# Kernel optimization log

Measured on AMD Instinct MI355X. Metric: run time of the kernel, lower is better.

## Reference

```python
import jax, jax.numpy as jnp
import numpy as np

N, Wd = 1000000, 20
EPS = 1e-16


def setup_inputs() -> dict:
    key = jax.random.key(0)
    ks = jax.random.split(key, 40)
    def rn(i, shape, scale=0.05):
        return jax.random.normal(ks[i], shape, dtype=jnp.float32) * scale
    inp = {
        "X": rn(0, (1, 14), 1.0),
        "read_weights": jax.nn.sigmoid(rn(1, (1, N), 1.0)),
        "write_weights": jax.nn.sigmoid(rn(2, (1, N), 1.0)),
        "Memory": jnp.full((N, Wd), 1e-6, dtype=jnp.float32),
        "read_head": jax.nn.sigmoid(rn(3, (1, Wd), 1.0)),
        "W1": rn(4, (48, 14)), "b1": rn(5, (48,)),
        "W2": rn(6, (72, 48)), "b2": rn(7, (72,)),
        "Wxi": rn(8, ((Wd + 6) * 2 + 2 * Wd, 72)), "bxi": rn(9, ((Wd + 6) * 2 + 2 * Wd,)),
        "Wz": rn(10, (3, 72)), "bz": rn(11, (3,)),
        "Wv": rn(12, (20, 325)), "bv": rn(13, (20,)),
        "aW1": rn(14, (110, 40)), "ab1": rn(15, (110,)),
        "aW2": rn(16, (190, 110)), "ab2": rn(17, (190,)),
        "aW3": rn(18, (270, 190)), "ab3": rn(19, (270,)),
        "aW4": rn(20, (325, 270)), "ab4": rn(21, (325,)),
        "mW1": rn(22, (110, 40)), "mb1": rn(23, (110,)),
        "mW2": rn(24, (190, 110)), "mb2": rn(25, (190,)),
        "mW3": rn(26, (270, 190)), "mb3": rn(27, (270,)),
        "mW4": rn(28, (325, 270)), "mb4": rn(29, (325,)),
    }
    return inp


def _alu(x, W1, b1, W2, b2, W3, b3, W4, b4):
    x = jax.nn.relu(x @ W1.T + b1)
    x = jax.nn.relu(x @ W2.T + b2)
    x = jax.nn.relu(x @ W3.T + b3)
    return jax.nn.softmax(x @ W4.T + b4, axis=-1)


def _head_params(p):  # p: (1, Wd+6)
    k = jnp.tanh(p[0, :Wd])[None, :]              # (1, Wd)
    g = jax.nn.sigmoid(p[0, Wd])
    s = jax.nn.softmax(p[0, Wd + 1:Wd + 4])        # (3,)
    gamma = 1.0 + jax.nn.softplus(p[0, Wd + 4])
    beta = jax.nn.softplus(p[0, Wd + 5])
    return k, g, s, gamma, beta


def _address(Memory, k, beta, g, s, gamma, w_prev):
    Me = Memory + EPS                              # (N, Wd)
    ke = k + EPS                                   # (1, Wd)
    num = (Me @ ke.T)[:, 0]                        # (N,)
    den = jnp.maximum(jnp.linalg.norm(Me, axis=-1), 1e-8) * \
          jnp.maximum(jnp.linalg.norm(ke, axis=-1), 1e-8)
    w_c = jax.nn.softmax((num / den) * beta)       # (N,)
    w_g = g * w_c + (1.0 - g) * w_prev             # (1, N)
    pad = jnp.concatenate([w_g[:, -1:], w_g, w_g[:, :1]], axis=1)  # (1, N+2)
    w_r = s[0] * pad[:, :N] + s[1] * pad[:, 1:N + 1] + s[2] * pad[:, 2:]
    w = w_r ** gamma
    return w / (jnp.sum(w, axis=1, keepdims=True) + EPS)


def reference(X, read_weights, write_weights, Memory, read_head,
              W1, b1, W2, b2, Wxi, bxi, Wz, bz, Wv, bv,
              aW1, ab1, aW2, ab2, aW3, ab3, aW4, ab4,
              mW1, mb1, mW2, mb2, mW3, mb3, mW4, mb4):
    h = X @ W1.T + b1                # (1, 48)  (no activation, faithful)
    h = h @ W2.T + b2                # (1, 72)
    xi = h @ Wxi.T + bxi             # (1, 92)
    zeta = h @ Wz.T + bz             # (1, 3)

    rp = xi[0, :Wd + 6][None, :]
    wp = xi[0, Wd + 6:(Wd + 6) * 2][None, :]
    erase = jax.nn.sigmoid(xi[0, (Wd + 6) * 2:(Wd + 6) * 2 + Wd][None, :])
    add = jnp.tanh(xi[0, (Wd + 6) * 2 + Wd:(Wd + 6) * 2 + 2 * Wd][None, :])

    k, g, s, gamma, beta = _head_params(rp)
    rw = _address(Memory, k, beta, g, s, gamma, read_weights)
    k, g, s, gamma, beta = _head_params(wp)
    ww = _address(Memory, k, beta, g, s, gamma, write_weights)

    new_read_head = rw @ Memory                    # (1, Wd)
    alu_in = jnp.concatenate([read_head, new_read_head], axis=1)  # (1, 2*Wd)

    rho = jax.nn.sigmoid(zeta[0, 0])
    alu_head = jax.nn.softmax(zeta[:, 1:], axis=-1)  # (1, 2)
    out_add = _alu(alu_in, aW1, ab1, aW2, ab2, aW3, ab3, aW4, ab4)
    out_mul = _alu(alu_in, mW1, mb1, mW2, mb2, mW3, mb3, mW4, mb4)
    out = alu_head[0, 0] * out_add + alu_head[0, 1] * out_mul  # (1, 325)

    v = out @ Wv.T + bv                              # (1, 20)
    add = rho * add + (1.0 - rho) * v

    new_memory = Memory * (1.0 - ww.T @ erase) + ww.T @ add  # (N, Wd)
    return out, rw, ww, new_memory, new_read_head
```

## Files before the change

kernel.cpp:

```cpp
#include <hip/hip_runtime.h>
#include <math.h>

#define NN 1000000
#define WD 20
#define NB 977
#define PST 1024

#define OUT_OFF 0
#define RW_OFF  325
#define WW_OFF  1000325
#define NM_OFF  2000325
#define NRH_OFF 22000325

__device__ __forceinline__ float sigmoidf_(float x){ return 1.0f/(1.0f+expf(-x)); }
__device__ __forceinline__ float softplusf_(float x){ return (x>30.f)?x:log1pf(expf(x)); }

__global__ void k_head(const float* __restrict__ X,
                       const float* __restrict__ W1, const float* __restrict__ b1,
                       const float* __restrict__ W2, const float* __restrict__ b2,
                       const float* __restrict__ Wxi, const float* __restrict__ bxi,
                       const float* __restrict__ Wz, const float* __restrict__ bz,
                       float* __restrict__ P){
  __shared__ float h1[48], h2[72], xi[92], zeta[3];
  int t = threadIdx.x;
  if(t<48){ float a=b1[t]; const float* w=W1+t*14; for(int c=0;c<14;c++) a+=X[c]*w[c]; h1[t]=a; }
  __syncthreads();
  if(t<72){ float a=b2[t]; const float* w=W2+t*48; for(int c=0;c<48;c++) a+=h1[c]*w[c]; h2[t]=a; }
  __syncthreads();
  if(t<92){ float a=bxi[t]; const float* w=Wxi+t*72; for(int c=0;c<72;c++) a+=h2[c]*w[c]; xi[t]=a; }
  else if(t<95){ int z=t-92; float a=bz[z]; const float* w=Wz+z*72; for(int c=0;c<72;c++) a+=h2[c]*w[c]; zeta[z]=a; }
  __syncthreads();
  if(t<20){
    P[0+t]  = tanhf(xi[t]);
    P[32+t] = tanhf(xi[26+t]);
    P[64+t] = sigmoidf_(xi[52+t]);
    P[84+t] = tanhf(xi[72+t]);
  }
  if(t==32){
    const float* p = xi;
    float g=sigmoidf_(p[20]);
    float a0=p[21],a1=p[22],a2=p[23];
    float mx=fmaxf(a0,fmaxf(a1,a2));
    float e0=expf(a0-mx),e1=expf(a1-mx),e2=expf(a2-mx),es=e0+e1+e2;
    float gamma=1.0f+softplusf_(p[24]);
    float beta=softplusf_(p[25]);
    float n2=0.f; for(int j=0;j<20;j++){ float ke=tanhf(p[j])+1e-16f; n2+=ke*ke; }
    P[20]=g; P[21]=e0/es; P[22]=e1/es; P[23]=e2/es; P[24]=gamma; P[25]=beta;
    P[26]=fmaxf(sqrtf(n2),1e-8f);
  }
  if(t==33){
    const float* p = xi+26;
    float g=sigmoidf_(p[20]);
    float a0=p[21],a1=p[22],a2=p[23];
    float mx=fmaxf(a0,fmaxf(a1,a2));
    float e0=expf(a0-mx),e1=expf(a1-mx),e2=expf(a2-mx),es=e0+e1+e2;
    float gamma=1.0f+softplusf_(p[24]);
    float beta=softplusf_(p[25]);
    float n2=0.f; for(int j=0;j<20;j++){ float ke=tanhf(p[j])+1e-16f; n2+=ke*ke; }
    P[52]=g; P[53]=e0/es; P[54]=e1/es; P[55]=e2/es; P[56]=gamma; P[57]=beta;
    P[58]=fmaxf(sqrtf(n2),1e-8f);
  }
  if(t==34){
    P[104]=sigmoidf_(zeta[0]);
    float mx=fmaxf(zeta[1],zeta[2]);
    float e1=expf(zeta[1]-mx), e2=expf(zeta[2]-mx);
    P[105]=e1/(e1+e2); P[106]=e2/(e1+e2);
  }
}

__global__ __launch_bounds__(256) void k_scores(const float* __restrict__ M, const float* __restrict__ P,
                         float* __restrict__ score_r, float* __restrict__ score_w,
                         float4* __restrict__ pms){
  int t=threadIdx.x, b=blockIdx.x;
  float kr[20], kw[20];
#pragma unroll
  for(int j=0;j<20;j++){ kr[j]=P[j]+1e-16f; kw[j]=P[32+j]+1e-16f; }
  float betar=P[25], betaw=P[57], knr=P[26], knw=P[58];
  float sR[4], sW[4];
#pragma unroll
  for(int p=0;p<4;p++){
    int i=b*1024+p*256+t;
    if(i<NN){
      const float4* row=(const float4*)(M+(size_t)i*WD);
      float dr=0.f,dw=0.f,n2=0.f;
#pragma unroll
      for(int q=0;q<5;q++){
        float4 v=row[q];
        float m0=v.x+1e-16f,m1=v.y+1e-16f,m2=v.z+1e-16f,m3=v.w+1e-16f;
        dr+=m0*kr[4*q]+m1*kr[4*q+1]+m2*kr[4*q+2]+m3*kr[4*q+3];
        dw+=m0*kw[4*q]+m1*kw[4*q+1]+m2*kw[4*q+2]+m3*kw[4*q+3];
        n2+=m0*m0+m1*m1+m2*m2+m3*m3;
      }
      float nm=fmaxf(sqrtf(n2),1e-8f);
      sR[p]=betar*(dr/(nm*knr));
      sW[p]=betaw*(dw/(nm*knw));
      score_r[i]=sR[p]; score_w[i]=sW[p];
    } else { sR[p]=-3.0e38f; sW[p]=-3.0e38f; }
  }
  __shared__ float r1[256], r2[256];
  __shared__ double d1[256], d2[256];
  float lm1=fmaxf(fmaxf(sR[0],sR[1]),fmaxf(sR[2],sR[3]));
  float lm2=fmaxf(fmaxf(sW[0],sW[1]),fmaxf(sW[2],sW[3]));
  r1[t]=lm1; r2[t]=lm2; __syncthreads();
  for(int o=128;o>0;o>>=1){ if(t<o){ r1[t]=fmaxf(r1[t],r1[t+o]); r2[t]=fmaxf(r2[t],r2[t+o]); } __syncthreads(); }
  float mb1=r1[0], mb2=r2[0]; __syncthreads();
  double s1=0.0,s2=0.0;
#pragma unroll
  for(int p=0;p<4;p++){ s1+=(double)expf(sR[p]-mb1); s2+=(double)expf(sW[p]-mb2); }
  d1[t]=s1; d2[t]=s2; __syncthreads();
  for(int o=128;o>0;o>>=1){ if(t<o){ d1[t]+=d1[t+o]; d2[t]+=d2[t+o]; } __syncthreads(); }
  if(t==0) pms[b]=make_float4(mb1,mb2,(float)d1[0],(float)d2[0]);
}

__global__ __launch_bounds__(256) void k_shift(const float* __restrict__ score_r, const float* __restrict__ score_w,
                        const float* __restrict__ wpr, const float* __restrict__ wpw,
                        const float* __restrict__ M, const float* __restrict__ P,
                        const float4* __restrict__ pms,
                        float* __restrict__ w_r_out, float* __restrict__ w_w_out,
                        double* __restrict__ pZ, double* __restrict__ pnrhT){
  __shared__ float r1[256], r2[256];
  __shared__ double d1[256], d2[256];
  __shared__ float bmS[4];
  __shared__ float wsum[4][20];
  int t=threadIdx.x, b=blockIdx.x;
  float4 v[4];
#pragma unroll
  for(int k=0;k<4;k++){
    int idx=t+k*256;
    v[k] = (idx<NB) ? pms[idx] : make_float4(-3.0e38f,-3.0e38f,0.f,0.f);
  }
  float lm1=fmaxf(fmaxf(v[0].x,v[1].x),fmaxf(v[2].x,v[3].x));
  float lm2=fmaxf(fmaxf(v[0].y,v[1].y),fmaxf(v[2].y,v[3].y));
  r1[t]=lm1; r2[t]=lm2; __syncthreads();
  for(int o=128;o>0;o>>=1){ if(t<o){ r1[t]=fmaxf(r1[t],r1[t+o]); r2[t]=fmaxf(r2[t],r2[t+o]); } __syncthreads(); }
  if(t==0){ bmS[0]=r1[0]; bmS[1]=r2[0]; } __syncthreads();
  float mr=bmS[0], mw=bmS[1];
  double s1=0.0,s2=0.0;
#pragma unroll
  for(int k=0;k<4;k++){
    s1 += (double)v[k].z * (double)expf(v[k].x-mr);
    s2 += (double)v[k].w * (double)expf(v[k].y-mw);
  }
  d1[t]=s1; d2[t]=s2; __syncthreads();
  for(int o=128;o>0;o>>=1){ if(t<o){ d1[t]+=d1[t+o]; d2[t]+=d2[t+o]; } __syncthreads(); }
  if(t==0){ bmS[2]=(float)d1[0]; bmS[3]=(float)d2[0]; } __syncthreads();
  float Sr=bmS[2], Sw=bmS[3];
  float gr=P[20], s0r=P[21], s1r=P[22], s2r=P[23], gar=P[24];
  float gw=P[52], s0w=P[53], s1w=P[54], s2w=P[55], gaw=P[56];
  float omgr=1.0f-gr, omgw=1.0f-gw;
  float acc[20];
#pragma unroll
  for(int j=0;j<20;j++) acc[j]=0.f;
  double zr=0.0, zw=0.0;
  for(int p=0;p<4;p++){
    int i=b*1024+p*256+t;
    if(i<NN){
      int im1=(i==0)?(NN-1):(i-1);
      int ip1=(i==NN-1)?0:(i+1);
      float wgrm = gr*(expf(score_r[im1]-mr)/Sr) + omgr*wpr[im1];
      float wgr0 = gr*(expf(score_r[i  ]-mr)/Sr) + omgr*wpr[i  ];
      float wgrp = gr*(expf(score_r[ip1]-mr)/Sr) + omgr*wpr[ip1];
      float wgwm = gw*(expf(score_w[im1]-mw)/Sw) + omgw*wpw[im1];
      float wgw0 = gw*(expf(score_w[i  ]-mw)/Sw) + omgw*wpw[i  ];
      float wgwp = gw*(expf(score_w[ip1]-mw)/Sw) + omgw*wpw[ip1];
      float wr = powf(s0r*wgrm + s1r*wgr0 + s2r*wgrp, gar);
      float ww = powf(s0w*wgwm + s1w*wgw0 + s2w*wgwp, gaw);
      w_r_out[i]=wr; w_w_out[i]=ww;
      zr+=(double)wr; zw+=(double)ww;
      const float4* row=(const float4*)(M+(size_t)i*WD);
#pragma unroll
      for(int q=0;q<5;q++){
        float4 mv=row[q];
        acc[4*q+0]+=wr*mv.x; acc[4*q+1]+=wr*mv.y; acc[4*q+2]+=wr*mv.z; acc[4*q+3]+=wr*mv.w;
      }
    }
  }
  d1[t]=zr; d2[t]=zw; __syncthreads();
  for(int o=128;o>0;o>>=1){ if(t<o){ d1[t]+=d1[t+o]; d2[t]+=d2[t+o]; } __syncthreads(); }
  if(t==0){ pZ[2*b]=d1[0]; pZ[2*b+1]=d2[0]; }
#pragma unroll
  for(int j=0;j<20;j++){
    for(int off=32;off>0;off>>=1) acc[j]+=__shfl_down(acc[j],off,64);
  }
  int wave=t>>6, lane=t&63;
  if(lane==0){
#pragma unroll
    for(int j=0;j<20;j++) wsum[wave][j]=acc[j];
  }
  __syncthreads();
  if(t<20){
    double s=(double)wsum[0][t]+(double)wsum[1][t]+(double)wsum[2][t]+(double)wsum[3][t];
    pnrhT[(size_t)t*PST+b]=s;
  }
}

__global__ __launch_bounds__(256) void k_nrh(const double* __restrict__ pZ, const double* __restrict__ pnrhT,
                      const float* __restrict__ read_head,
                      float* __restrict__ in40, float* __restrict__ out, double* __restrict__ Sd){
  __shared__ double dd[256];
  __shared__ double bZ[2];
  int t=threadIdx.x, j=blockIdx.x;
  double a=0.0,c=0.0;
  for(int idx=t; idx<NB; idx+=256){ a+=pZ[2*idx]; c+=pZ[2*idx+1]; }
  dd[t]=a; __syncthreads();
  for(int o=128;o>0;o>>=1){ if(t<o) dd[t]+=dd[t+o]; __syncthreads(); }
  if(t==0) bZ[0]=dd[0]; __syncthreads();
  dd[t]=c; __syncthreads();
  for(int o=128;o>0;o>>=1){ if(t<o) dd[t]+=dd[t+o]; __syncthreads(); }
  if(t==0) bZ[1]=dd[0]; __syncthreads();
  if(j==0 && t==0){ Sd[0]=bZ[0]; Sd[1]=bZ[1]; }
  double s=0.0;
  for(int idx=t; idx<NB; idx+=256) s+=pnrhT[(size_t)j*PST+idx];
  dd[t]=s; __syncthreads();
  for(int o=128;o>0;o>>=1){ if(t<o) dd[t]+=dd[t+o]; __syncthreads(); }
  if(t==0){
    float nv=(float)(dd[0]/(bZ[0]+1e-16));
    in40[20+j]=nv; out[NRH_OFF+j]=nv;
    in40[j]=read_head[j];
  }
}

__global__ __launch_bounds__(256) void k_layer(const float* __restrict__ Wa, const float* __restrict__ ba,
                        const float* __restrict__ Wm, const float* __restrict__ bm,
                        const float* __restrict__ inA, const float* __restrict__ inM,
                        float* __restrict__ oA, float* __restrict__ oM,
                        int rows, int K, int RB, int doRelu){
  int net = (blockIdx.x >= RB) ? 1 : 0;
  const float* W = net ? Wm : Wa;
  const float* bb = net ? bm : ba;
  const float* in = net ? inM : inA;
  float* o = net ? oM : oA;
  int wave=threadIdx.x>>6, lane=threadIdx.x&63;
  int r=(blockIdx.x - net*RB)*4 + wave;
  if(r>=rows) return;
  const float* w = W + (size_t)r*K;
  float a=0.f;
  for(int c=lane; c<K; c+=64) a += w[c]*in[c];
  for(int off=32;off>0;off>>=1) a += __shfl_down(a,off,64);
  if(lane==0){
    float vv=a+bb[r];
    o[r]= doRelu ? fmaxf(vv,0.f) : vv;
  }
}

__global__ __launch_bounds__(512) void k_fin(const float* __restrict__ h4a, const float* __restrict__ h4m,
                      const float* __restrict__ Wv, const float* __restrict__ bv,
                      float* __restrict__ P, float* __restrict__ out){
  __shared__ float red[512];
  __shared__ float A[325], B[325];
  __shared__ float sc[2];
  int t=threadIdx.x;
  float la=(t<325)?h4a[t]:-3.0e38f;
  red[t]=la; __syncthreads();
  for(int o=256;o>0;o>>=1){ if(t<o) red[t]=fmaxf(red[t],red[t+o]); __syncthreads(); }
  if(t==0) sc[0]=red[0]; __syncthreads();
  float ea=(t<325)?expf(la-sc[0]):0.f;
  red[t]=ea; __syncthreads();
  for(int o=256;o>0;o>>=1){ if(t<o) red[t]+=red[t+o]; __syncthreads(); }
  if(t==0) sc[1]=red[0]; __syncthreads();
  if(t<325) A[t]=ea/sc[1];
  __syncthreads();
  float lm=(t<325)?h4m[t]:-3.0e38f;
  red[t]=lm; __syncthreads();
  for(int o=256;o>0;o>>=1){ if(t<o) red[t]=fmaxf(red[t],red[t+o]); __syncthreads(); }
  if(t==0) sc[0]=red[0]; __syncthreads();
  float em=(t<325)?expf(lm-sc[0]):0.f;
  red[t]=em; __syncthreads();
  for(int o=256;o>0;o>>=1){ if(t<o) red[t]+=red[t+o]; __syncthreads(); }
  if(t==0) sc[1]=red[0]; __syncthreads();
  if(t<325) B[t]=em/sc[1];
  __syncthreads();
  float ah0=P[105], ah1=P[106];
  if(t<325){ float ov=ah0*A[t]+ah1*B[t]; out[OUT_OFF+t]=ov; A[t]=ov; }
  __syncthreads();
  int wave=t>>6, lane=t&63;
  for(int r=wave; r<20; r+=8){
    const float* w=Wv+(size_t)r*325;
    float a=0.f;
    for(int c=lane;c<325;c+=64) a+=w[c]*A[c];
    for(int off=32;off>0;off>>=1) a+=__shfl_down(a,off,64);
    if(lane==0){
      float vv=a+bv[r];
      float rho=P[104];
      P[112+r]=rho*P[84+r]+(1.0f-rho)*vv;
    }
  }
}

__global__ __launch_bounds__(256) void k_memupd(const float* __restrict__ M,
                         float* __restrict__ w_r, float* __restrict__ w_w,
                         const float* __restrict__ P, const double* __restrict__ Sd,
                         float* __restrict__ nm){
  int t=threadIdx.x, b=blockIdx.x;
  float er[20], af[20];
#pragma unroll
  for(int j=0;j<20;j++){ er[j]=P[64+j]; af[j]=P[112+j]; }
  float Zr=(float)Sd[0]+1e-16f, Zw=(float)Sd[1]+1e-16f;
  for(int p=0;p<4;p++){
    int i=b*1024+p*256+t;
    if(i<NN){
      float wrn=w_r[i]/Zr;
      float wwn=w_w[i]/Zw;
      w_r[i]=wrn; w_w[i]=wwn;
      const float4* row=(const float4*)(M+(size_t)i*WD);
      float4* dst=(float4*)(nm+(size_t)i*WD);
#pragma unroll
      for(int q=0;q<5;q++){
        float4 v=row[q];
        float4 o;
        o.x=v.x*(1.0f-wwn*er[4*q+0])+wwn*af[4*q+0];
        o.y=v.y*(1.0f-wwn*er[4*q+1])+wwn*af[4*q+1];
        o.z=v.z*(1.0f-wwn*er[4*q+2])+wwn*af[4*q+2];
        o.w=v.w*(1.0f-wwn*er[4*q+3])+wwn*af[4*q+3];
        dst[q]=o;
      }
    }
  }
}

extern "C" void kernel_launch(void* const* d_in, const int* in_sizes, int n_in,
                              void* d_out, int out_size, void* d_ws, size_t ws_size,
                              hipStream_t stream) {
  const float* X    =(const float*)d_in[0];
  const float* rwp  =(const float*)d_in[1];
  const float* wwp  =(const float*)d_in[2];
  const float* Mem  =(const float*)d_in[3];
  const float* rhd  =(const float*)d_in[4];
  const float* W1   =(const float*)d_in[5];
  const float* b1   =(const float*)d_in[6];
  const float* W2   =(const float*)d_in[7];
  const float* b2   =(const float*)d_in[8];
  const float* Wxi  =(const float*)d_in[9];
  const float* bxi  =(const float*)d_in[10];
  const float* Wz   =(const float*)d_in[11];
  const float* bz   =(const float*)d_in[12];
  const float* Wv   =(const float*)d_in[13];
  const float* bv   =(const float*)d_in[14];
  const float* aW1  =(const float*)d_in[15];
  const float* ab1  =(const float*)d_in[16];
  const float* aW2  =(const float*)d_in[17];
  const float* ab2  =(const float*)d_in[18];
  const float* aW3  =(const float*)d_in[19];
  const float* ab3  =(const float*)d_in[20];
  const float* aW4  =(const float*)d_in[21];
  const float* ab4  =(const float*)d_in[22];
  const float* mW1  =(const float*)d_in[23];
  const float* mb1  =(const float*)d_in[24];
  const float* mW2  =(const float*)d_in[25];
  const float* mb2  =(const float*)d_in[26];
  const float* mW3  =(const float*)d_in[27];
  const float* mb3  =(const float*)d_in[28];
  const float* mW4  =(const float*)d_in[29];
  const float* mb4  =(const float*)d_in[30];

  float* out = (float*)d_out;
  char* ws = (char*)d_ws;
  float*  P     = (float*) (ws + 0);
  float4* pms   = (float4*)(ws + 4096);
  double* pZ    = (double*)(ws + 32768);
  double* pnrhT = (double*)(ws + 65536);
  double* Sd    = (double*)(ws + 229376);
  float*  in40  = (float*) (ws + 229504);
  float*  F     = (float*) (ws + 229760);
  float *h1a=F,      *h1m=F+110;
  float *h2a=F+220,  *h2m=F+410;
  float *h3a=F+600,  *h3m=F+870;
  float *h4a=F+1140, *h4m=F+1465;

  float* score_r = out + NM_OFF;
  float* score_w = score_r + NN;
  float* w_r = out + RW_OFF;
  float* w_w = out + WW_OFF;
  float* nm  = out + NM_OFF;

  k_head<<<1,128,0,stream>>>(X,W1,b1,W2,b2,Wxi,bxi,Wz,bz,P);
  k_scores<<<NB,256,0,stream>>>(Mem,P,score_r,score_w,pms);
  k_shift<<<NB,256,0,stream>>>(score_r,score_w,rwp,wwp,Mem,P,pms,w_r,w_w,pZ,pnrhT);
  k_nrh<<<20,256,0,stream>>>(pZ,pnrhT,rhd,in40,out,Sd);
  k_layer<<<56,256,0,stream>>>(aW1,ab1,mW1,mb1,in40,in40,h1a,h1m,110,40,28,1);
  k_layer<<<96,256,0,stream>>>(aW2,ab2,mW2,mb2,h1a,h1m,h2a,h2m,190,110,48,1);
  k_layer<<<136,256,0,stream>>>(aW3,ab3,mW3,mb3,h2a,h2m,h3a,h3m,270,190,68,1);
  k_layer<<<164,256,0,stream>>>(aW4,ab4,mW4,mb4,h3a,h3m,h4a,h4m,325,270,82,0);
  k_fin<<<1,512,0,stream>>>(h4a,h4m,Wv,bv,P,out);
  k_memupd<<<NB,256,0,stream>>>(Mem,w_r,w_w,P,Sd,nm);
}
```

Before: 120.5 us.

## Stage memory rows through LDS, interleave scores, fuse MLP chain with grid barriers

Memory rows are now loaded cooperatively as coalesced float4 tiles into shared memory in the scores, shift and update kernels, replacing per-thread strided 80-byte row reads. The update kernel also writes its output back through LDS. Read and write scores are stored interleaved as float2, so the shift stencil fetches both with one load. The reduction, four MLP layers and final projection are merged into one persistent 96-block kernel using atomic global barriers, removing six launches at the risk of spin-wait cost and a deadlock if not all blocks are co-resident.

```diff
diff --git a/kernel.cpp b/kernel.cpp
--- a/kernel.cpp
+++ b/kernel.cpp
@@ -2,9 +2,11 @@
 #include <math.h>
 
 #define NN 1000000
+#define NF4 5000000
 #define WD 20
 #define NB 977
 #define PST 1024
+#define MLPB 96
 
 #define OUT_OFF 0
 #define RW_OFF  325
@@ -15,14 +17,25 @@
 __device__ __forceinline__ float sigmoidf_(float x){ return 1.0f/(1.0f+expf(-x)); }
 __device__ __forceinline__ float softplusf_(float x){ return (x>30.f)?x:log1pf(expf(x)); }
 
+__device__ __forceinline__ void gbar(unsigned* c, unsigned nb){
+  __syncthreads();
+  if(threadIdx.x==0){
+    __hip_atomic_fetch_add(c,1u,__ATOMIC_ACQ_REL,__HIP_MEMORY_SCOPE_AGENT);
+    while(__hip_atomic_load(c,__ATOMIC_ACQUIRE,__HIP_MEMORY_SCOPE_AGENT) < nb)
+      __builtin_amdgcn_s_sleep(8);
+  }
+  __syncthreads();
+}
+
 __global__ void k_head(const float* __restrict__ X,
                        const float* __restrict__ W1, const float* __restrict__ b1,
                        const float* __restrict__ W2, const float* __restrict__ b2,
                        const float* __restrict__ Wxi, const float* __restrict__ bxi,
                        const float* __restrict__ Wz, const float* __restrict__ bz,
-                       float* __restrict__ P){
+                       float* __restrict__ P, unsigned* __restrict__ cnt){
   __shared__ float h1[48], h2[72], xi[92], zeta[3];
   int t = threadIdx.x;
+  if(t>=96 && t<112) cnt[t-96]=0u;
   if(t<48){ float a=b1[t]; const float* w=W1+t*14; for(int c=0;c<14;c++) a+=X[c]*w[c]; h1[t]=a; }
   __syncthreads();
   if(t<72){ float a=b2[t]; const float* w=W2+t*48; for(int c=0;c<48;c++) a+=h1[c]*w[c]; h2[t]=a; }
@@ -69,36 +82,46 @@
 }
 
 __global__ __launch_bounds__(256) void k_scores(const float* __restrict__ M, const float* __restrict__ P,
-                         float* __restrict__ score_r, float* __restrict__ score_w,
-                         float4* __restrict__ pms){
+                         float2* __restrict__ sc2, float4* __restrict__ pms){
+  __shared__ float4 ld[1280];
   int t=threadIdx.x, b=blockIdx.x;
   float kr[20], kw[20];
 #pragma unroll
   for(int j=0;j<20;j++){ kr[j]=P[j]+1e-16f; kw[j]=P[32+j]+1e-16f; }
   float betar=P[25], betaw=P[57], knr=P[26], knw=P[58];
+  const float4* Mf4=(const float4*)M;
   float sR[4], sW[4];
-#pragma unroll
   for(int p=0;p<4;p++){
-    int i=b*1024+p*256+t;
+    int rb=b*1024+p*256;
+    size_t f4b=(size_t)rb*5;
+#pragma unroll
+    for(int k=0;k<5;k++){
+      size_t idx=f4b+(size_t)(k*256+t);
+      ld[k*256+t] = (idx<NF4)?Mf4[idx]:make_float4(0.f,0.f,0.f,0.f);
+    }
+    __syncthreads();
+    int i=rb+t;
+    float srv=-3.0e38f, swv=-3.0e38f;
     if(i<NN){
-      const float4* row=(const float4*)(M+(size_t)i*WD);
       float dr=0.f,dw=0.f,n2=0.f;
 #pragma unroll
       for(int q=0;q<5;q++){
-        float4 v=row[q];
+        float4 v=ld[t*5+q];
         float m0=v.x+1e-16f,m1=v.y+1e-16f,m2=v.z+1e-16f,m3=v.w+1e-16f;
         dr+=m0*kr[4*q]+m1*kr[4*q+1]+m2*kr[4*q+2]+m3*kr[4*q+3];
         dw+=m0*kw[4*q]+m1*kw[4*q+1]+m2*kw[4*q+2]+m3*kw[4*q+3];
         n2+=m0*m0+m1*m1+m2*m2+m3*m3;
       }
       float nm=fmaxf(sqrtf(n2),1e-8f);
-      sR[p]=betar*(dr/(nm*knr));
-      sW[p]=betaw*(dw/(nm*knw));
-      score_r[i]=sR[p]; score_w[i]=sW[p];
-    } else { sR[p]=-3.0e38f; sW[p]=-3.0e38f; }
-  }
-  __shared__ float r1[256], r2[256];
-  __shared__ double d1[256], d2[256];
+      srv=betar*(dr/(nm*knr));
+      swv=betaw*(dw/(nm*knw));
+      sc2[i]=make_float2(srv,swv);
+    }
+    sR[p]=srv; sW[p]=swv;
+    __syncthreads();
+  }
+  float* r1=(float*)ld; float* r2=r1+256;
+  double* d1=(double*)(r1+512); double* d2=d1+256;
   float lm1=fmaxf(fmaxf(sR[0],sR[1]),fmaxf(sR[2],sR[3]));
   float lm2=fmaxf(fmaxf(sW[0],sW[1]),fmaxf(sW[2],sW[3]));
   r1[t]=lm1; r2[t]=lm2; __syncthreads();
@@ -112,25 +135,26 @@
   if(t==0) pms[b]=make_float4(mb1,mb2,(float)d1[0],(float)d2[0]);
 }
 
-__global__ __launch_bounds__(256) void k_shift(const float* __restrict__ score_r, const float* __restrict__ score_w,
+__global__ __launch_bounds__(256) void k_shift(const float2* __restrict__ sc2,
                         const float* __restrict__ wpr, const float* __restrict__ wpw,
                         const float* __restrict__ M, const float* __restrict__ P,
                         const float4* __restrict__ pms,
                         float* __restrict__ w_r_out, float* __restrict__ w_w_out,
                         double* __restrict__ pZ, double* __restrict__ pnrhT){
-  __shared__ float r1[256], r2[256];
-  __shared__ double d1[256], d2[256];
+  __shared__ float4 ld[1280];
   __shared__ float bmS[4];
-  __shared__ float wsum[4][20];
+  float* r1=(float*)ld; float* r2=r1+256;
+  double* d1=(double*)(r1+512); double* d2=d1+256;
+  float* wsum=(float*)(d2+256);
   int t=threadIdx.x, b=blockIdx.x;
-  float4 v[4];
+  float4 v4[4];
 #pragma unroll
   for(int k=0;k<4;k++){
     int idx=t+k*256;
-    v[k] = (idx<NB) ? pms[idx] : make_float4(-3.0e38f,-3.0e38f,0.f,0.f);
-  }
-  float lm1=fmaxf(fmaxf(v[0].x,v[1].x),fmaxf(v[2].x,v[3].x));
-  float lm2=fmaxf(fmaxf(v[0].y,v[1].y),fmaxf(v[2].y,v[3].y));
+    v4[k] = (idx<NB) ? pms[idx] : make_float4(-3.0e38f,-3.0e38f,0.f,0.f);
+  }
+  float lm1=fmaxf(fmaxf(v4[0].x,v4[1].x),fmaxf(v4[2].x,v4[3].x));
+  float lm2=fmaxf(fmaxf(v4[0].y,v4[1].y),fmaxf(v4[2].y,v4[3].y));
   r1[t]=lm1; r2[t]=lm2; __syncthreads();
   for(int o=128;o>0;o>>=1){ if(t<o){ r1[t]=fmaxf(r1[t],r1[t+o]); r2[t]=fmaxf(r2[t],r2[t+o]); } __syncthreads(); }
   if(t==0){ bmS[0]=r1[0]; bmS[1]=r2[0]; } __syncthreads();
@@ -138,8 +162,8 @@
   double s1=0.0,s2=0.0;
 #pragma unroll
   for(int k=0;k<4;k++){
-    s1 += (double)v[k].z * (double)expf(v[k].x-mr);
-    s2 += (double)v[k].w * (double)expf(v[k].y-mw);
+    s1 += (double)v4[k].z * (double)expf(v4[k].x-mr);
+    s2 += (double)v4[k].w * (double)expf(v4[k].y-mw);
   }
   d1[t]=s1; d2[t]=s2; __syncthreads();
   for(int o=128;o>0;o>>=1){ if(t<o){ d1[t]+=d1[t+o]; d2[t]+=d2[t+o]; } __syncthreads(); }
@@ -148,36 +172,47 @@
   float gr=P[20], s0r=P[21], s1r=P[22], s2r=P[23], gar=P[24];
   float gw=P[52], s0w=P[53], s1w=P[54], s2w=P[55], gaw=P[56];
   float omgr=1.0f-gr, omgw=1.0f-gw;
+  const float4* Mf4=(const float4*)M;
   float acc[20];
 #pragma unroll
   for(int j=0;j<20;j++) acc[j]=0.f;
   double zr=0.0, zw=0.0;
   for(int p=0;p<4;p++){
-    int i=b*1024+p*256+t;
+    int rb=b*1024+p*256;
+    size_t f4b=(size_t)rb*5;
+#pragma unroll
+    for(int k=0;k<5;k++){
+      size_t idx=f4b+(size_t)(k*256+t);
+      ld[k*256+t] = (idx<NF4)?Mf4[idx]:make_float4(0.f,0.f,0.f,0.f);
+    }
+    __syncthreads();
+    int i=rb+t;
     if(i<NN){
       int im1=(i==0)?(NN-1):(i-1);
       int ip1=(i==NN-1)?0:(i+1);
-      float wgrm = gr*(expf(score_r[im1]-mr)/Sr) + omgr*wpr[im1];
-      float wgr0 = gr*(expf(score_r[i  ]-mr)/Sr) + omgr*wpr[i  ];
-      float wgrp = gr*(expf(score_r[ip1]-mr)/Sr) + omgr*wpr[ip1];
-      float wgwm = gw*(expf(score_w[im1]-mw)/Sw) + omgw*wpw[im1];
-      float wgw0 = gw*(expf(score_w[i  ]-mw)/Sw) + omgw*wpw[i  ];
-      float wgwp = gw*(expf(score_w[ip1]-mw)/Sw) + omgw*wpw[ip1];
+      float2 scm=sc2[im1], sc0=sc2[i], scp=sc2[ip1];
+      float wgrm = gr*(expf(scm.x-mr)/Sr) + omgr*wpr[im1];
+      float wgr0 = gr*(expf(sc0.x-mr)/Sr) + omgr*wpr[i  ];
+      float wgrp = gr*(expf(scp.x-mr)/Sr) + omgr*wpr[ip1];
+      float wgwm = gw*(expf(scm.y-mw)/Sw) + omgw*wpw[im1];
+      float wgw0 = gw*(expf(sc0.y-mw)/Sw) + omgw*wpw[i  ];
+      float wgwp = gw*(expf(scp.y-mw)/Sw) + omgw*wpw[ip1];
       float wr = powf(s0r*wgrm + s1r*wgr0 + s2r*wgrp, gar);
       float ww = powf(s0w*wgwm + s1w*wgw0 + s2w*wgwp, gaw);
       w_r_out[i]=wr; w_w_out[i]=ww;
       zr+=(double)wr; zw+=(double)ww;
-      const float4* row=(const float4*)(M+(size_t)i*WD);
 #pragma unroll
       for(int q=0;q<5;q++){
-        float4 mv=row[q];
+        float4 mv=ld[t*5+q];
         acc[4*q+0]+=wr*mv.x; acc[4*q+1]+=wr*mv.y; acc[4*q+2]+=wr*mv.z; acc[4*q+3]+=wr*mv.w;
       }
     }
+    __syncthreads();
   }
   d1[t]=zr; d2[t]=zw; __syncthreads();
   for(int o=128;o>0;o>>=1){ if(t<o){ d1[t]+=d1[t+o]; d2[t]+=d2[t+o]; } __syncthreads(); }
   if(t==0){ pZ[2*b]=d1[0]; pZ[2*b+1]=d2[0]; }
+  __syncthreads();
 #pragma unroll
   for(int j=0;j<20;j++){
     for(int off=32;off>0;off>>=1) acc[j]+=__shfl_down(acc[j],off,64);
@@ -185,104 +220,143 @@
   int wave=t>>6, lane=t&63;
   if(lane==0){
 #pragma unroll
-    for(int j=0;j<20;j++) wsum[wave][j]=acc[j];
+    for(int j=0;j<20;j++) wsum[wave*20+j]=acc[j];
   }
   __syncthreads();
   if(t<20){
-    double s=(double)wsum[0][t]+(double)wsum[1][t]+(double)wsum[2][t]+(double)wsum[3][t];
+    double s=(double)wsum[0*20+t]+(double)wsum[1*20+t]+(double)wsum[2*20+t]+(double)wsum[3*20+t];
     pnrhT[(size_t)t*PST+b]=s;
   }
 }
 
-__global__ __launch_bounds__(256) void k_nrh(const double* __restrict__ pZ, const double* __restrict__ pnrhT,
+__global__ __launch_bounds__(256) void k_mlp(const double* __restrict__ pZ, const double* __restrict__ pnrhT,
                       const float* __restrict__ read_head,
-                      float* __restrict__ in40, float* __restrict__ out, double* __restrict__ Sd){
+                      const float* __restrict__ aW1,const float* __restrict__ ab1,
+                      const float* __restrict__ aW2,const float* __restrict__ ab2,
+                      const float* __restrict__ aW3,const float* __restrict__ ab3,
+                      const float* __restrict__ aW4,const float* __restrict__ ab4,
+                      const float* __restrict__ mW1,const float* __restrict__ mb1,
+                      const float* __restrict__ mW2,const float* __restrict__ mb2,
+                      const float* __restrict__ mW3,const float* __restrict__ mb3,
+                      const float* __restrict__ mW4,const float* __restrict__ mb4,
+                      const float* __restrict__ Wv, const float* __restrict__ bv,
+                      float* __restrict__ P, float* __restrict__ out,
+                      float* __restrict__ in40, float* __restrict__ F,
+                      double* __restrict__ Sd, unsigned* __restrict__ cnt){
   __shared__ double dd[256];
-  __shared__ double bZ[2];
-  int t=threadIdx.x, j=blockIdx.x;
-  double a=0.0,c=0.0;
-  for(int idx=t; idx<NB; idx+=256){ a+=pZ[2*idx]; c+=pZ[2*idx+1]; }
-  dd[t]=a; __syncthreads();
-  for(int o=128;o>0;o>>=1){ if(t<o) dd[t]+=dd[t+o]; __syncthreads(); }
-  if(t==0) bZ[0]=dd[0]; __syncthreads();
-  dd[t]=c; __syncthreads();
-  for(int o=128;o>0;o>>=1){ if(t<o) dd[t]+=dd[t+o]; __syncthreads(); }
-  if(t==0) bZ[1]=dd[0]; __syncthreads();
-  if(j==0 && t==0){ Sd[0]=bZ[0]; Sd[1]=bZ[1]; }
-  double s=0.0;
-  for(int idx=t; idx<NB; idx+=256) s+=pnrhT[(size_t)j*PST+idx];
-  dd[t]=s; __syncthreads();
-  for(int o=128;o>0;o>>=1){ if(t<o) dd[t]+=dd[t+o]; __syncthreads(); }
-  if(t==0){
-    float nv=(float)(dd[0]/(bZ[0]+1e-16));
-    in40[20+j]=nv; out[NRH_OFF+j]=nv;
-    in40[j]=read_head[j];
-  }
-}
-
-__global__ __launch_bounds__(256) void k_layer(const float* __restrict__ Wa, const float* __restrict__ ba,
-                        const float* __restrict__ Wm, const float* __restrict__ bm,
-                        const float* __restrict__ inA, const float* __restrict__ inM,
-                        float* __restrict__ oA, float* __restrict__ oM,
-                        int rows, int K, int RB, int doRelu){
-  int net = (blockIdx.x >= RB) ? 1 : 0;
-  const float* W = net ? Wm : Wa;
-  const float* bb = net ? bm : ba;
-  const float* in = net ? inM : inA;
-  float* o = net ? oM : oA;
-  int wave=threadIdx.x>>6, lane=threadIdx.x&63;
-  int r=(blockIdx.x - net*RB)*4 + wave;
-  if(r>=rows) return;
-  const float* w = W + (size_t)r*K;
-  float a=0.f;
-  for(int c=lane; c<K; c+=64) a += w[c]*in[c];
-  for(int off=32;off>0;off>>=1) a += __shfl_down(a,off,64);
-  if(lane==0){
-    float vv=a+bb[r];
-    o[r]= doRelu ? fmaxf(vv,0.f) : vv;
-  }
-}
-
-__global__ __launch_bounds__(512) void k_fin(const float* __restrict__ h4a, const float* __restrict__ h4m,
-                      const float* __restrict__ Wv, const float* __restrict__ bv,
-                      float* __restrict__ P, float* __restrict__ out){
-  __shared__ float red[512];
-  __shared__ float A[325], B[325];
-  __shared__ float sc[2];
-  int t=threadIdx.x;
-  float la=(t<325)?h4a[t]:-3.0e38f;
-  red[t]=la; __syncthreads();
-  for(int o=256;o>0;o>>=1){ if(t<o) red[t]=fmaxf(red[t],red[t+o]); __syncthreads(); }
-  if(t==0) sc[0]=red[0]; __syncthreads();
-  float ea=(t<325)?expf(la-sc[0]):0.f;
-  red[t]=ea; __syncthreads();
-  for(int o=256;o>0;o>>=1){ if(t<o) red[t]+=red[t+o]; __syncthreads(); }
-  if(t==0) sc[1]=red[0]; __syncthreads();
-  if(t<325) A[t]=ea/sc[1];
-  __syncthreads();
-  float lm=(t<325)?h4m[t]:-3.0e38f;
-  red[t]=lm; __syncthreads();
-  for(int o=256;o>0;o>>=1){ if(t<o) red[t]=fmaxf(red[t],red[t+o]); __syncthreads(); }
-  if(t==0) sc[0]=red[0]; __syncthreads();
-  float em=(t<325)?expf(lm-sc[0]):0.f;
-  red[t]=em; __syncthreads();
-  for(int o=256;o>0;o>>=1){ if(t<o) red[t]+=red[t+o]; __syncthreads(); }
-  if(t==0) sc[1]=red[0]; __syncthreads();
-  if(t<325) B[t]=em/sc[1];
-  __syncthreads();
-  float ah0=P[105], ah1=P[106];
-  if(t<325){ float ov=ah0*A[t]+ah1*B[t]; out[OUT_OFF+t]=ov; A[t]=ov; }
-  __syncthreads();
-  int wave=t>>6, lane=t&63;
-  for(int r=wave; r<20; r+=8){
-    const float* w=Wv+(size_t)r*325;
-    float a=0.f;
-    for(int c=lane;c<325;c+=64) a+=w[c]*A[c];
+  __shared__ float A[325], B[325], red[256], sc[2];
+  int t=threadIdx.x, b=blockIdx.x;
+  int wid=b*4+(t>>6), lane=t&63;
+  float *h1a=F,      *h1m=F+110;
+  float *h2a=F+220,  *h2m=F+410;
+  float *h3a=F+600,  *h3m=F+870;
+  float *h4a=F+1140, *h4m=F+1465;
+  if(b<20){
+    double a=0.0;
+    for(int idx=t; idx<NB; idx+=256) a+=pZ[2*idx];
+    dd[t]=a; __syncthreads();
+    for(int o=128;o>0;o>>=1){ if(t<o) dd[t]+=dd[t+o]; __syncthreads(); }
+    double Zr=dd[0]; __syncthreads();
+    double c=0.0;
+    for(int idx=t; idx<NB; idx+=256) c+=pnrhT[(size_t)b*PST+idx];
+    dd[t]=c; __syncthreads();
+    for(int o=128;o>0;o>>=1){ if(t<o) dd[t]+=dd[t+o]; __syncthreads(); }
+    if(t==0){
+      float nv=(float)(dd[0]/(Zr+1e-16));
+      in40[20+b]=nv; out[NRH_OFF+b]=nv;
+    }
+  } else if(b==20){
+    double a=0.0,c=0.0;
+    for(int idx=t; idx<NB; idx+=256){ a+=pZ[2*idx]; c+=pZ[2*idx+1]; }
+    dd[t]=a; __syncthreads();
+    for(int o=128;o>0;o>>=1){ if(t<o) dd[t]+=dd[t+o]; __syncthreads(); }
+    if(t==0) Sd[0]=dd[0];
+    __syncthreads();
+    dd[t]=c; __syncthreads();
+    for(int o=128;o>0;o>>=1){ if(t<o) dd[t]+=dd[t+o]; __syncthreads(); }
+    if(t==0) Sd[1]=dd[0];
+  } else if(b==21){
+    if(t<20) in40[t]=read_head[t];
+  }
+  gbar(cnt+0,MLPB);
+  if(wid<220){
+    int net=(wid>=110), r=wid-net*110;
+    const float* W=net?mW1:aW1; const float* bb=net?mb1:ab1; float* o=net?h1m:h1a;
+    const float* w=W+(size_t)r*40;
+    float a=0.f; for(int c=lane;c<40;c+=64) a+=w[c]*in40[c];
     for(int off=32;off>0;off>>=1) a+=__shfl_down(a,off,64);
-    if(lane==0){
-      float vv=a+bv[r];
-      float rho=P[104];
-      P[112+r]=rho*P[84+r]+(1.0f-rho)*vv;
+    if(lane==0) o[r]=fmaxf(a+bb[r],0.f);
+  }
+  gbar(cnt+1,MLPB);
+  if(wid<380){
+    int net=(wid>=190), r=wid-net*190;
+    const float* W=net?mW2:aW2; const float* bb=net?mb2:ab2;
+    const float* in=net?h1m:h1a; float* o=net?h2m:h2a;
+    const float* w=W+(size_t)r*110;
+    float a=0.f; for(int c=lane;c<110;c+=64) a+=w[c]*in[c];
+    for(int off=32;off>0;off>>=1) a+=__shfl_down(a,off,64);
+    if(lane==0) o[r]=fmaxf(a+bb[r],0.f);
+  }
+  gbar(cnt+2,MLPB);
+  for(int r0=wid; r0<540; r0+=MLPB*4){
+    int net=(r0>=270), r=r0-net*270;
+    const float* W=net?mW3:aW3; const float* bb=net?mb3:ab3;
+    const float* in=net?h2m:h2a; float* o=net?h3m:h3a;
+    const float* w=W+(size_t)r*190;
+    float a=0.f; for(int c=lane;c<190;c+=64) a+=w[c]*in[c];
+    for(int off=32;off>0;off>>=1) a+=__shfl_down(a,off,64);
+    if(lane==0) o[r]=fmaxf(a+bb[r],0.f);
+  }
+  gbar(cnt+3,MLPB);
+  for(int r0=wid; r0<650; r0+=MLPB*4){
+    int net=(r0>=325), r=r0-net*325;
+    const float* W=net?mW4:aW4; const float* bb=net?mb4:ab4;
+    const float* in=net?h3m:h3a; float* o=net?h4m:h4a;
+    const float* w=W+(size_t)r*270;
+    float a=0.f; for(int c=lane;c<270;c+=64) a+=w[c]*in[c];
+    for(int off=32;off>0;off>>=1) a+=__shfl_down(a,off,64);
+    if(lane==0) o[r]=a+bb[r];
+  }
+  gbar(cnt+4,MLPB);
+  if(b==0){
+    float x0=h4a[t];
+    float x1=(t<69)?h4a[256+t]:-3.0e38f;
+    red[t]=fmaxf(x0,x1); __syncthreads();
+    for(int o=128;o>0;o>>=1){ if(t<o) red[t]=fmaxf(red[t],red[t+o]); __syncthreads(); }
+    if(t==0) sc[0]=red[0]; __syncthreads();
+    float e0=expf(x0-sc[0]), e1=(t<69)?expf(x1-sc[0]):0.f;
+    red[t]=e0+e1; __syncthreads();
+    for(int o=128;o>0;o>>=1){ if(t<o) red[t]+=red[t+o]; __syncthreads(); }
+    if(t==0) sc[1]=red[0]; __syncthreads();
+    A[t]=e0/sc[1]; if(t<69) A[256+t]=e1/sc[1];
+    __syncthreads();
+    float y0=h4m[t];
+    float y1=(t<69)?h4m[256+t]:-3.0e38f;
+    red[t]=fmaxf(y0,y1); __syncthreads();
+    for(int o=128;o>0;o>>=1){ if(t<o) red[t]=fmaxf(red[t],red[t+o]); __syncthreads(); }
+    if(t==0) sc[0]=red[0]; __syncthreads();
+    float f0=expf(y0-sc[0]), f1=(t<69)?expf(y1-sc[0]):0.f;
+    red[t]=f0+f1; __syncthreads();
+    for(int o=128;o>0;o>>=1){ if(t<o) red[t]+=red[t+o]; __syncthreads(); }
+    if(t==0) sc[1]=red[0]; __syncthreads();
+    B[t]=f0/sc[1]; if(t<69) B[256+t]=f1/sc[1];
+    __syncthreads();
+    float ah0=P[105], ah1=P[106];
+    float ov0=ah0*A[t]+ah1*B[t];
+    out[OUT_OFF+t]=ov0; A[t]=ov0;
+    if(t<69){ float ov1=ah0*A[256+t]+ah1*B[256+t]; out[OUT_OFF+256+t]=ov1; A[256+t]=ov1; }
+    __syncthreads();
+    int wv=t>>6;
+    float rho=P[104];
+    for(int r=wv; r<20; r+=4){
+      const float* w=Wv+(size_t)r*325;
+      float a=0.f;
+      for(int c=lane;c<325;c+=64) a+=w[c]*A[c];
+      for(int off=32;off>0;off>>=1) a+=__shfl_down(a,off,64);
+      if(lane==0){
+        float vv=a+bv[r];
+        P[112+r]=rho*P[84+r]+(1.0f-rho)*vv;
+      }
     }
   }
 }
@@ -291,30 +365,46 @@
                          float* __restrict__ w_r, float* __restrict__ w_w,
                          const float* __restrict__ P, const double* __restrict__ Sd,
                          float* __restrict__ nm){
+  __shared__ float4 ld[1280];
   int t=threadIdx.x, b=blockIdx.x;
   float er[20], af[20];
 #pragma unroll
   for(int j=0;j<20;j++){ er[j]=P[64+j]; af[j]=P[112+j]; }
   float Zr=(float)Sd[0]+1e-16f, Zw=(float)Sd[1]+1e-16f;
+  const float4* Mf4=(const float4*)M;
+  float4* nmf4=(float4*)nm;
   for(int p=0;p<4;p++){
-    int i=b*1024+p*256+t;
+    int rb=b*1024+p*256;
+    size_t f4b=(size_t)rb*5;
+#pragma unroll
+    for(int k=0;k<5;k++){
+      size_t idx=f4b+(size_t)(k*256+t);
+      if(idx<NF4) ld[k*256+t]=Mf4[idx];
+    }
+    __syncthreads();
+    int i=rb+t;
     if(i<NN){
       float wrn=w_r[i]/Zr;
       float wwn=w_w[i]/Zw;
       w_r[i]=wrn; w_w[i]=wwn;
-      const float4* row=(const float4*)(M+(size_t)i*WD);
-      float4* dst=(float4*)(nm+(size_t)i*WD);
 #pragma unroll
       for(int q=0;q<5;q++){
-        float4 v=row[q];
+        float4 v=ld[t*5+q];
         float4 o;
         o.x=v.x*(1.0f-wwn*er[4*q+0])+wwn*af[4*q+0];
         o.y=v.y*(1.0f-wwn*er[4*q+1])+wwn*af[4*q+1];
         o.z=v.z*(1.0f-wwn*er[4*q+2])+wwn*af[4*q+2];
         o.w=v.w*(1.0f-wwn*er[4*q+3])+wwn*af[4*q+3];
-        dst[q]=o;
+        ld[t*5+q]=o;
       }
     }
+    __syncthreads();
+#pragma unroll
+    for(int k=0;k<5;k++){
+      size_t idx=f4b+(size_t)(k*256+t);
+      if(idx<NF4) nmf4[idx]=ld[k*256+t];
+    }
+    __syncthreads();
   }
 }
 
@@ -355,32 +445,26 @@
 
   float* out = (float*)d_out;
   char* ws = (char*)d_ws;
-  float*  P     = (float*) (ws + 0);
-  float4* pms   = (float4*)(ws + 4096);
-  double* pZ    = (double*)(ws + 32768);
-  double* pnrhT = (double*)(ws + 65536);
-  double* Sd    = (double*)(ws + 229376);
-  float*  in40  = (float*) (ws + 229504);
-  float*  F     = (float*) (ws + 229760);
-  float *h1a=F,      *h1m=F+110;
-  float *h2a=F+220,  *h2m=F+410;
-  float *h3a=F+600,  *h3m=F+870;
-  float *h4a=F+1140, *h4m=F+1465;
-
-  float* score_r = out + NM_OFF;
-  float* score_w = score_r + NN;
-  float* w_r = out + RW_OFF;
-  float* w_w = out + WW_OFF;
-  float* nm  = out + NM_OFF;
-
-  k_head<<<1,128,0,stream>>>(X,W1,b1,W2,b2,Wxi,bxi,Wz,bz,P);
-  k_scores<<<NB,256,0,stream>>>(Mem,P,score_r,score_w,pms);
-  k_shift<<<NB,256,0,stream>>>(score_r,score_w,rwp,wwp,Mem,P,pms,w_r,w_w,pZ,pnrhT);
-  k_nrh<<<20,256,0,stream>>>(pZ,pnrhT,rhd,in40,out,Sd);
-  k_layer<<<56,256,0,stream>>>(aW1,ab1,mW1,mb1,in40,in40,h1a,h1m,110,40,28,1);
-  k_layer<<<96,256,0,stream>>>(aW2,ab2,mW2,mb2,h1a,h1m,h2a,h2m,190,110,48,1);
-  k_layer<<<136,256,0,stream>>>(aW3,ab3,mW3,mb3,h2a,h2m,h3a,h3m,270,190,68,1);
-  k_layer<<<164,256,0,stream>>>(aW4,ab4,mW4,mb4,h3a,h3m,h4a,h4m,325,270,82,0);
-  k_fin<<<1,512,0,stream>>>(h4a,h4m,Wv,bv,P,out);
+  float*    P     = (float*)   (ws + 0);
+  unsigned* cnt   = (unsigned*)(ws + 1024);
+  double*   Sd    = (double*)  (ws + 2048);
+  float*    in40  = (float*)   (ws + 2304);
+  float*    F     = (float*)   (ws + 4096);
+  float4*   pms   = (float4*)  (ws + 16384);
+  double*   pZ    = (double*)  (ws + 32768);
+  double*   pnrhT = (double*)  (ws + 65536);
+
+  float2* sc2 = (float2*)(out + NM_OFF);
+  float*  w_r = out + RW_OFF;
+  float*  w_w = out + WW_OFF;
+  float*  nm  = out + NM_OFF;
+
+  k_head<<<1,128,0,stream>>>(X,W1,b1,W2,b2,Wxi,bxi,Wz,bz,P,cnt);
+  k_scores<<<NB,256,0,stream>>>(Mem,P,sc2,pms);
+  k_shift<<<NB,256,0,stream>>>(sc2,rwp,wwp,Mem,P,pms,w_r,w_w,pZ,pnrhT);
+  k_mlp<<<MLPB,256,0,stream>>>(pZ,pnrhT,rhd,
+                               aW1,ab1,aW2,ab2,aW3,ab3,aW4,ab4,
+                               mW1,mb1,mW2,mb2,mW3,mb3,mW4,mb4,
+                               Wv,bv,P,out,in40,F,Sd,cnt);
   k_memupd<<<NB,256,0,stream>>>(Mem,w_r,w_w,P,Sd,nm);
 }
```

After: 141.7 us. +17.6%, slower.
